# Optimization experiments

Hardware: AMD Instinct MI355X
Metric: run time of the kernel (lower is better)

Reference implementation:

```python
import jax, jax.numpy as jnp
import numpy as np

B, IN, E, H, V, T = 512, 256, 256, 512, 32000, 32


def setup_inputs() -> dict:
    key = jax.random.key(0)
    ks = jax.random.split(key, 8)
    s = 0.05
    return {
        "x": jax.random.normal(ks[0], (B, IN), jnp.float32),
        "agent_w": jax.random.normal(ks[1], (H, IN), jnp.float32) * s,
        "agent_b": jnp.zeros((H,), jnp.float32),
        "sos": jax.random.normal(ks[2], (E,), jnp.float32) * 0.01,
        "emb": jax.random.normal(ks[3], (V, E), jnp.float32) * s,
        "W_ih": jax.random.normal(ks[4], (3 * H, E), jnp.float32) * s,
        "W_hh": jax.random.normal(ks[5], (3 * H, H), jnp.float32) * s,
        "b_ih": jnp.zeros((3 * H,), jnp.float32),
        "b_hh": jnp.zeros((3 * H,), jnp.float32),
        "W_out": jax.random.normal(ks[6], (V, H), jnp.float32) * s,
        "b_out": jnp.zeros((V,), jnp.float32),
        "W_stop": jax.random.normal(ks[7], (1, H), jnp.float32) * s,
        "b_stop": jnp.zeros((1,), jnp.float32),
    }


def _gru_cell(inp, h, W_ih, W_hh, b_ih, b_hh):
    gi = inp @ W_ih.T + b_ih              # [B, 3H]
    gh = h @ W_hh.T + b_hh                # [B, 3H]
    i_r, i_z, i_n = jnp.split(gi, 3, axis=1)
    h_r, h_z, h_n = jnp.split(gh, 3, axis=1)
    r = jax.nn.sigmoid(i_r + h_r)
    z = jax.nn.sigmoid(i_z + h_z)
    n = jnp.tanh(i_n + r * h_n)
    return (1.0 - z) * n + z * h


def reference(x, agent_w, agent_b, sos, emb, W_ih, W_hh, b_ih, b_hh,
              W_out, b_out, W_stop, b_stop):
    h0 = x @ agent_w.T + agent_b                       # agent(x) -> [B, H]
    inp0 = jnp.broadcast_to(sos, (x.shape[0], sos.shape[0]))
    keys = jax.random.split(jax.random.key(42), T)

    def step(carry, k):
        h, inp = carry
        h = _gru_cell(inp, h, W_ih, W_hh, b_ih, b_hh)  # noise_scale=0 -> no noise
        symb_logits = h @ W_out.T + b_out              # [B, V]
        stop_logit = (h @ W_stop.T + b_stop)[:, 0]     # [B]
        logp = jax.nn.log_softmax(symb_logits, axis=1)
        k1, k2 = jax.random.split(k)
        symb = jax.random.categorical(k1, symb_logits, axis=1)          # [B] int
        p_stop = jax.nn.sigmoid(stop_logit)
        stop = jax.random.bernoulli(k2, p_stop).astype(jnp.float32)     # [B]
        symb_lp = jnp.take_along_axis(logp, symb[:, None], axis=1)[:, 0]
        # Bernoulli: log p = s - softplus(s), log(1-p) = -softplus(s)
        sp = jax.nn.softplus(stop_logit)
        stop_lp = stop * stop_logit - sp
        symb_ent = -jnp.sum(jnp.exp(logp) * logp, axis=1)
        stop_ent = sp - stop_logit * p_stop
        inp_next = emb[symb]
        return (h, inp_next), (symb, stop, symb_lp, stop_lp, symb_ent, stop_ent)

    _, ys = jax.lax.scan(step, (h0, inp0), keys)
    symb_seq, stop_seq, symb_lp, stop_lp, symb_ent, stop_ent = ys
    # [T, B] -> [B, T]
    tr = lambda a: a.T
    return (tr(symb_seq), tr(stop_seq).astype(jnp.int32),
            tr(symb_lp), tr(stop_lp), tr(symb_ent), tr(stop_ent))
```

## Files before the change

### kernel.cpp

```cpp
#include <hip/hip_runtime.h>
#include <hip/hip_bf16.h>
#include <stdint.h>

#define JAX_PARTITIONABLE 1

#define Bz 512
#define INz 256
#define Ez 256
#define Hz 512
#define Vz 32000
#define Tz 32
#define BTz (Bz * Tz)
#define TINYF 1.17549435e-38f

typedef float otype;
__device__ __forceinline__ void store_out(otype* out, int idx, float v) {
  out[idx] = v;
}

__device__ __forceinline__ uint32_t rotl32(uint32_t x, int r) {
  return (x << r) | (x >> (32 - r));
}
__device__ __forceinline__ void threefry2x32(uint32_t k0, uint32_t k1,
                                             uint32_t x0, uint32_t x1,
                                             uint32_t& o0, uint32_t& o1) {
  const uint32_t ks2 = k0 ^ k1 ^ 0x1BD11BDAu;
  x0 += k0; x1 += k1;
#define TF_R4(a, b, c, d)                              \
  x0 += x1; x1 = rotl32(x1, a); x1 ^= x0;              \
  x0 += x1; x1 = rotl32(x1, b); x1 ^= x0;              \
  x0 += x1; x1 = rotl32(x1, c); x1 ^= x0;              \
  x0 += x1; x1 = rotl32(x1, d); x1 ^= x0;
  TF_R4(13, 15, 26, 6)  x0 += k1;  x1 += ks2 + 1u;
  TF_R4(17, 29, 16, 24) x0 += ks2; x1 += k0 + 2u;
  TF_R4(13, 15, 26, 6)  x0 += k0;  x1 += k1 + 3u;
  TF_R4(17, 29, 16, 24) x0 += k1;  x1 += ks2 + 4u;
  TF_R4(13, 15, 26, 6)  x0 += ks2; x1 += k0 + 5u;
#undef TF_R4
  o0 = x0; o1 = x1;
}
__device__ __forceinline__ uint32_t rand_bits32(uint32_t ka, uint32_t kb,
                                                uint32_t idx, uint32_t n) {
#if JAX_PARTITIONABLE
  (void)n;
  uint32_t o0, o1;
  threefry2x32(ka, kb, 0u, idx, o0, o1);
  return o0 ^ o1;
#else
  uint32_t half = n >> 1;
  uint32_t o0, o1;
  if (idx < half) { threefry2x32(ka, kb, idx, idx + half, o0, o1); return o0; }
  threefry2x32(ka, kb, idx - half, idx, o0, o1); return o1;
#endif
}
__device__ __forceinline__ float bits_to_f01(uint32_t bits) {
  return __uint_as_float((bits >> 9) | 0x3f800000u) - 1.0f;
}

__global__ void RnnSenderReinforce_36799279792759_kernel(otype* __restrict__ out,
                                                         int n, float v) {
  int i = blockIdx.x * 256 + threadIdx.x;
  if (i < n) out[i] = v;
}

__global__ void keys_kernel(uint32_t* __restrict__ keys) {
  int t = threadIdx.x;
  if (t >= Tz) return;
  uint32_t ka, kb;
#if JAX_PARTITIONABLE
  threefry2x32(0u, 42u, 0u, (uint32_t)t, ka, kb);
#else
  {
    uint32_t j0 = 2u * t, j1 = 2u * t + 1u;
    uint32_t a0, a1, b0, b1;
    if (j0 < Tz) { threefry2x32(0u, 42u, j0, j0 + Tz, a0, a1); ka = a0; }
    else         { threefry2x32(0u, 42u, j0 - Tz, j0, a0, a1); ka = a1; }
    if (j1 < Tz) { threefry2x32(0u, 42u, j1, j1 + Tz, b0, b1); kb = b0; }
    else         { threefry2x32(0u, 42u, j1 - Tz, j1, b0, b1); kb = b1; }
  }
#endif
  uint32_t o0, o1;
#if JAX_PARTITIONABLE
  threefry2x32(ka, kb, 0u, 0u, o0, o1);
  keys[t * 4 + 0] = o0; keys[t * 4 + 1] = o1;
  threefry2x32(ka, kb, 0u, 1u, o0, o1);
  keys[t * 4 + 2] = o0; keys[t * 4 + 3] = o1;
#else
  uint32_t p0, p1, q0, q1;
  threefry2x32(ka, kb, 0u, 2u, p0, p1);
  threefry2x32(ka, kb, 1u, 3u, q0, q1);
  keys[t * 4 + 0] = p0; keys[t * 4 + 1] = q0;
  keys[t * 4 + 2] = p1; keys[t * 4 + 3] = q1;
#endif
}

#define GBM 64
#define GBN 64
#define GBK 32
#define LDSS 68

__device__ __forceinline__ void gemm_bt_body(const float* __restrict__ A,
                                             const float* __restrict__ W,
                                             const float* __restrict__ bias,
                                             float* __restrict__ C,
                                             int M, int N, int K,
                                             int bx, int by,
                                             float* As, float* Bs) {
  const int tid = threadIdx.x;
  const int tx = tid & 15;
  const int ty = tid >> 4;
  const int m0 = by * GBM;
  const int n0 = bx * GBN;
  const int lr = tid >> 3;
  const int lc = (tid & 7) << 2;

  float acc[4][4] = {};
  const float* Ap = A + (size_t)(m0 + lr) * K + lc;
  const float* Wp = W + (size_t)(n0 + lr) * K + lc;
  const size_t rstep = (size_t)32 * K;

  for (int k0 = 0; k0 < K; k0 += GBK) {
    float4 a0 = *(const float4*)(Ap + k0);
    float4 a1 = *(const float4*)(Ap + k0 + rstep);
    float4 b0 = *(const float4*)(Wp + k0);
    float4 b1 = *(const float4*)(Wp + k0 + rstep);
    __syncthreads();
    As[(lc + 0) * LDSS + lr] = a0.x;
    As[(lc + 1) * LDSS + lr] = a0.y;
    As[(lc + 2) * LDSS + lr] = a0.z;
    As[(lc + 3) * LDSS + lr] = a0.w;
    As[(lc + 0) * LDSS + lr + 32] = a1.x;
    As[(lc + 1) * LDSS + lr + 32] = a1.y;
    As[(lc + 2) * LDSS + lr + 32] = a1.z;
    As[(lc + 3) * LDSS + lr + 32] = a1.w;
    Bs[(lc + 0) * LDSS + lr] = b0.x;
    Bs[(lc + 1) * LDSS + lr] = b0.y;
    Bs[(lc + 2) * LDSS + lr] = b0.z;
    Bs[(lc + 3) * LDSS + lr] = b0.w;
    Bs[(lc + 0) * LDSS + lr + 32] = b1.x;
    Bs[(lc + 1) * LDSS + lr + 32] = b1.y;
    Bs[(lc + 2) * LDSS + lr + 32] = b1.z;
    Bs[(lc + 3) * LDSS + lr + 32] = b1.w;
    __syncthreads();
#pragma unroll
    for (int kk = 0; kk < GBK; kk++) {
      float4 af = *(const float4*)&As[kk * LDSS + (ty << 2)];
      float4 bf = *(const float4*)&Bs[kk * LDSS + (tx << 2)];
      float ar[4] = {af.x, af.y, af.z, af.w};
      float br[4] = {bf.x, bf.y, bf.z, bf.w};
#pragma unroll
      for (int i = 0; i < 4; i++)
#pragma unroll
        for (int j = 0; j < 4; j++)
          acc[i][j] = fmaf(ar[i], br[j], acc[i][j]);
    }
  }

  const int nc = n0 + (tx << 2);
  float4 bv;
  bv.x = bias[nc + 0]; bv.y = bias[nc + 1]; bv.z = bias[nc + 2]; bv.w = bias[nc + 3];
#pragma unroll
  for (int i = 0; i < 4; i++) {
    int m = m0 + (ty << 2) + i;
    float4 o;
    o.x = acc[i][0] + bv.x;
    o.y = acc[i][1] + bv.y;
    o.z = acc[i][2] + bv.z;
    o.w = acc[i][3] + bv.w;
    *(float4*)(C + (size_t)m * N + nc) = o;
  }
}

__global__ __launch_bounds__(256) void gemm_bt(const float* __restrict__ A,
                                               const float* __restrict__ W,
                                               const float* __restrict__ bias,
                                               float* __restrict__ C,
                                               int M, int N, int K) {
  __shared__ __align__(16) float As[GBK * LDSS];
  __shared__ __align__(16) float Bs[GBK * LDSS];
  gemm_bt_body(A, W, bias, C, M, N, K, blockIdx.x, blockIdx.y, As, Bs);
}

__global__ __launch_bounds__(256) void gru2_kernel(const float* __restrict__ inp,
                                                   const float* __restrict__ Wih,
                                                   const float* __restrict__ bih,
                                                   float* __restrict__ gi,
                                                   const float* __restrict__ h,
                                                   const float* __restrict__ Whh,
                                                   const float* __restrict__ bhh,
                                                   float* __restrict__ gh) {
  __shared__ __align__(16) float As[GBK * LDSS];
  __shared__ __align__(16) float Bs[GBK * LDSS];
  if (blockIdx.z == 0)
    gemm_bt_body(inp, Wih, bih, gi, Bz, 3 * Hz, Ez, blockIdx.x, blockIdx.y, As, Bs);
  else
    gemm_bt_body(h, Whh, bhh, gh, Bz, 3 * Hz, Hz, blockIdx.x, blockIdx.y, As, Bs);
}

#define QBM 256
#define QBN 128
#define QBK 32
#define QLDA 260
#define QLDB 132

__global__ __launch_bounds__(256, 2) void gemm256_bt(const float* __restrict__ A,
                                                     const float* __restrict__ W,
                                                     const float* __restrict__ bias,
                                                     float* __restrict__ C,
                                                     int M, int N, int K) {
  __shared__ __align__(16) float As[QBK * QLDA];
  __shared__ __align__(16) float Bs[QBK * QLDB];
  const int tid = threadIdx.x;
  const int tx = tid & 15;
  const int ty = tid >> 4;

  const int nP = N / QBN;
  const int G = nP >> 3;
  const int lim = G << 4;
  int b = blockIdx.x;
  int P, mi;
  if (b < lim) {
    int g = b >> 4, r = b & 15;
    mi = r >> 3;
    P = (g << 3) + (r & 7);
  } else {
    int e = b - lim;
    P = (G << 3) + (e & 1);
    mi = e >> 1;
  }
  const int m0 = mi * QBM;
  const int n0 = P * QBN;

  const float* Ap = A + (size_t)(m0 + tid) * K;
  const int brr = tid >> 1;
  const int bk = (tid & 1) << 4;
  const float* Wp = W + (size_t)(n0 + brr) * K + bk;

  float4 a[8], bb[4];
#pragma unroll
  for (int j = 0; j < 8; j++) a[j] = *(const float4*)(Ap + j * 4);
#pragma unroll
  for (int j = 0; j < 4; j++) bb[j] = *(const float4*)(Wp + j * 4);

  float acc[16][8] = {};

  for (int k0 = 0; k0 < K; k0 += QBK) {
    __syncthreads();
#pragma unroll
    for (int j = 0; j < 8; j++) {
      As[(j * 4 + 0) * QLDA + tid] = a[j].x;
      As[(j * 4 + 1) * QLDA + tid] = a[j].y;
      As[(j * 4 + 2) * QLDA + tid] = a[j].z;
      As[(j * 4 + 3) * QLDA + tid] = a[j].w;
    }
#pragma unroll
    for (int j = 0; j < 4; j++) {
      Bs[(bk + j * 4 + 0) * QLDB + brr] = bb[j].x;
      Bs[(bk + j * 4 + 1) * QLDB + brr] = bb[j].y;
      Bs[(bk + j * 4 + 2) * QLDB + brr] = bb[j].z;
      Bs[(bk + j * 4 + 3) * QLDB + brr] = bb[j].w;
    }
    __syncthreads();
    if (k0 + QBK < K) {
#pragma unroll
      for (int j = 0; j < 8; j++)
        a[j] = *(const float4*)(Ap + k0 + QBK + j * 4);
#pragma unroll
      for (int j = 0; j < 4; j++)
        bb[j] = *(const float4*)(Wp + k0 + QBK + j * 4);
    }
#pragma unroll 2
    for (int kk = 0; kk < QBK; kk++) {
      const float* Ar = &As[kk * QLDA + (ty << 2)];
      float4 xa0 = *(const float4*)(Ar);
      float4 xa1 = *(const float4*)(Ar + 64);
      float4 xa2 = *(const float4*)(Ar + 128);
      float4 xa3 = *(const float4*)(Ar + 192);
      float4 xb0 = *(const float4*)&Bs[kk * QLDB + (tx << 2)];
      float4 xb1 = *(const float4*)&Bs[kk * QLDB + 64 + (tx << 2)];
      float am[16] = {xa0.x, xa0.y, xa0.z, xa0.w, xa1.x, xa1.y, xa1.z, xa1.w,
                      xa2.x, xa2.y, xa2.z, xa2.w, xa3.x, xa3.y, xa3.z, xa3.w};
      float bn[8] = {xb0.x, xb0.y, xb0.z, xb0.w, xb1.x, xb1.y, xb1.z, xb1.w};
#pragma unroll
      for (int i = 0; i < 16; i++)
#pragma unroll
        for (int j = 0; j < 8; j++)
          acc[i][j] = fmaf(am[i], bn[j], acc[i][j]);
    }
  }

  const int nc0 = n0 + (tx << 2);
  const float4 bv0 = *(const float4*)(bias + nc0);
  const float4 bv1 = *(const float4*)(bias + nc0 + 64);
#pragma unroll
  for (int q = 0; q < 4; q++) {
#pragma unroll
    for (int i = 0; i < 4; i++) {
      const int m = m0 + q * 64 + (ty << 2) + i;
      float* Cp = C + (size_t)m * N + nc0;
      float4 o;
      o.x = acc[q * 4 + i][0] + bv0.x;
      o.y = acc[q * 4 + i][1] + bv0.y;
      o.z = acc[q * 4 + i][2] + bv0.z;
      o.w = acc[q * 4 + i][3] + bv0.w;
      *(float4*)Cp = o;
      float4 o2;
      o2.x = acc[q * 4 + i][4] + bv1.x;
      o2.y = acc[q * 4 + i][5] + bv1.y;
      o2.z = acc[q * 4 + i][6] + bv1.z;
      o2.w = acc[q * 4 + i][7] + bv1.w;
      *(float4*)(Cp + 64) = o2;
    }
  }
}

__global__ __launch_bounds__(512) void gates_stop_kernel(
    const float* __restrict__ gi, const float* __restrict__ gh,
    float* __restrict__ h, const float* __restrict__ W_stop,
    const float* __restrict__ b_stop, const uint32_t* __restrict__ keys,
    int t, otype* __restrict__ out) {
  __shared__ float hrow[Hz];
  const int b = blockIdx.x;
  const int j = threadIdx.x;
  const float* gib = gi + (size_t)b * (3 * Hz);
  const float* ghb = gh + (size_t)b * (3 * Hz);
  float ir = gib[j], iz = gib[j + Hz], in_ = gib[j + 2 * Hz];
  float hr = ghb[j], hz = ghb[j + Hz], hn = ghb[j + 2 * Hz];
  float r = 1.0f / (1.0f + expf(-(ir + hr)));
  float z = 1.0f / (1.0f + expf(-(iz + hz)));
  float n = tanhf(in_ + r * hn);
  float hv = h[(size_t)b * Hz + j];
  float hnew = (1.0f - z) * n + z * hv;
  h[(size_t)b * Hz + j] = hnew;
  hrow[j] = hnew;
  __syncthreads();
  if (j < 64) {
    const int lane = j;
    float s = 0.0f;
    for (int k = lane; k < Hz; k += 64) s = fmaf(hrow[k], W_stop[k], s);
#pragma unroll
    for (int off = 32; off; off >>= 1) s += __shfl_down(s, off, 64);
    if (lane == 0) {
      s += b_stop[0];
      uint32_t bits = rand_bits32(keys[t * 4 + 2], keys[t * 4 + 3], (uint32_t)b, Bz);
      float u = bits_to_f01(bits);
      float p = 1.0f / (1.0f + expf(-s));
      float stop = (u < p) ? 1.0f : 0.0f;
      float sp = fmaxf(s, 0.0f) + log1pf(expf(-fabsf(s)));
      store_out(out, 1 * BTz + b * Tz + t, stop);
      store_out(out, 3 * BTz + b * Tz + t, stop * s - sp);
      store_out(out, 5 * BTz + b * Tz + t, sp - s * p);
    }
  }
}

__global__ __launch_bounds__(256) void sample_kernel(const float* __restrict__ logits,
                                                     const uint32_t* __restrict__ keys,
                                                     int t, otype* __restrict__ out,
                                                     const float* __restrict__ emb,
                                                     float* __restrict__ inp) {
  __shared__ float sm[256], sg[256], sgl[256], sz[256], ss[256];
  __shared__ int sgi[256];
  __shared__ int ssymb;
  const int tid = threadIdx.x;
  const int b = blockIdx.x;
  const float* lb = logits + (size_t)b * Vz;
  const uint32_t k1a = keys[t * 4 + 0], k1b = keys[t * 4 + 1];
  const uint32_t base = (uint32_t)b * (uint32_t)Vz;

  float m = -INFINITY, gbest = -INFINITY, glogit = 0.0f;
  int gidx = 0x7FFFFFFF;
  for (int v = tid; v < Vz; v += 256) {
    float l = lb[v];
    m = fmaxf(m, l);
    uint32_t bits = rand_bits32(k1a, k1b, base + (uint32_t)v, (uint32_t)Bz * Vz);
    float f = bits_to_f01(bits);
    float u = fmaxf(TINYF, f + TINYF);
    float g = -logf(-logf(u));
    float val = l + g;
    if (val > gbest) { gbest = val; gidx = v; glogit = l; }
  }
  sm[tid] = m; sg[tid] = gbest; sgi[tid] = gidx; sgl[tid] = glogit;
  __syncthreads();
  for (int s2 = 128; s2; s2 >>= 1) {
    if (tid < s2) {
      sm[tid] = fmaxf(sm[tid], sm[tid + s2]);
      float go = sg[tid + s2]; int io = sgi[tid + s2];
      if (go > sg[tid] || (go == sg[tid] && io < sgi[tid])) {
        sg[tid] = go; sgi[tid] = io; sgl[tid] = sgl[tid + s2];
      }
    }
    __syncthreads();
  }
  const float M = sm[0];

  float Z = 0.0f, S1 = 0.0f;
  for (int v = tid; v < Vz; v += 256) {
    float sft = lb[v] - M;
    float e = expf(sft);
    Z += e;
    S1 = fmaf(e, sft, S1);
  }
  sz[tid] = Z; ss[tid] = S1;
  __syncthreads();
  for (int s2 = 128; s2; s2 >>= 1) {
    if (tid < s2) { sz[tid] += sz[tid + s2]; ss[tid] += ss[tid + s2]; }
    __syncthreads();
  }
  if (tid == 0) {
    float Zt = sz[0], S1t = ss[0];
    float lse = logf(Zt);
    int symb = sgi[0];
    store_out(out, 0 * BTz + b * Tz + t, (float)symb);
    store_out(out, 2 * BTz + b * Tz + t, (sgl[0] - M) - lse);
    store_out(out, 4 * BTz + b * Tz + t, lse - S1t / Zt);
    ssymb = symb;
  }
  __syncthreads();
  int s = ssymb;
  s = (s < 0) ? 0 : ((s >= Vz) ? (Vz - 1) : s);
  inp[(size_t)b * Ez + tid] = emb[(size_t)s * Ez + tid];
}

__global__ void init_inp_kernel(float* __restrict__ inp, const float* __restrict__ sos) {
  inp[blockIdx.x * Ez + threadIdx.x] = sos[threadIdx.x];
}

extern "C" __attribute__((visibility("default")))
void kernel_launch(void* const* d_in, const int* in_sizes, int n_in,
                   void* d_out, int out_size, void* d_ws, size_t ws_size,
                   hipStream_t stream) {
  const float* x       = (const float*)d_in[0];
  const float* agent_w = (const float*)d_in[1];
  const float* agent_b = (const float*)d_in[2];
  const float* sos     = (const float*)d_in[3];
  const float* emb     = (const float*)d_in[4];
  const float* W_ih    = (const float*)d_in[5];
  const float* W_hh    = (const float*)d_in[6];
  const float* b_ih    = (const float*)d_in[7];
  const float* b_hh    = (const float*)d_in[8];
  const float* W_out   = (const float*)d_in[9];
  const float* b_out   = (const float*)d_in[10];
  const float* W_stop  = (const float*)d_in[11];
  const float* b_stop  = (const float*)d_in[12];
  otype* out = (otype*)d_out;

  float* ws = (float*)d_ws;
  float* h      = ws;
  float* inp    = h + (size_t)Bz * Hz;
  float* gi     = inp + (size_t)Bz * Ez;
  float* gh     = gi + (size_t)Bz * 3 * Hz;
  float* logits = gh + (size_t)Bz * 3 * Hz;
  uint32_t* keys = (uint32_t*)(logits + (size_t)Bz * Vz);

  keys_kernel<<<1, 64, 0, stream>>>(keys);
  init_inp_kernel<<<Bz, Ez, 0, stream>>>(inp, sos);
  gemm_bt<<<dim3(Hz / GBN, Bz / GBM), 256, 0, stream>>>(x, agent_w, agent_b, h,
                                                        Bz, Hz, INz);
  for (int t = 0; t < Tz; t++) {
    gru2_kernel<<<dim3(3 * Hz / GBN, Bz / GBM, 2), 256, 0, stream>>>(
        inp, W_ih, b_ih, gi, h, W_hh, b_hh, gh);
    gates_stop_kernel<<<Bz, 512, 0, stream>>>(gi, gh, h, W_stop, b_stop, keys,
                                              t, out);
    gemm256_bt<<<(Vz / QBN) * (Bz / QBM), 256, 0, stream>>>(h, W_out, b_out,
                                                            logits, Bz, Vz, Hz);
    sample_kernel<<<Bz, 256, 0, stream>>>(logits, keys, t, out, emb, inp);
  }
}
```

Before: 11.12 ms.

## Replace output-projection GEMM with 128x128 double-buffered LDS tile kernel

The vocabulary-projection GEMM moves from 256x128 tiles with 256 threads and 128 accumulators per thread to 128x128 tiles with 512 threads, 32 accumulators per thread, and double-buffered shared memory. The aim is higher occupancy and overlap of global loads and LDS staging with FMA work, using one barrier per K-step. In exchange each block reuses less data from its tile, so more global and LDS traffic flows per FLOP. The block-to-tile swizzle is hardcoded for these problem dimensions.

```diff
diff --git a/kernel.cpp b/kernel.cpp
--- a/kernel.cpp
+++ b/kernel.cpp
@@ -197,120 +197,119 @@
     gemm_bt_body(h, Whh, bhh, gh, Bz, 3 * Hz, Hz, blockIdx.x, blockIdx.y, As, Bs);
 }
 
-#define QBM 256
-#define QBN 128
-#define QBK 32
-#define QLDA 260
-#define QLDB 132
-
-__global__ __launch_bounds__(256, 2) void gemm256_bt(const float* __restrict__ A,
+#define DBM 128
+#define DBN 128
+#define DBK 32
+#define DLD 132
+
+__global__ __launch_bounds__(512, 4) void gemm128_db(const float* __restrict__ A,
                                                      const float* __restrict__ W,
                                                      const float* __restrict__ bias,
                                                      float* __restrict__ C,
                                                      int M, int N, int K) {
-  __shared__ __align__(16) float As[QBK * QLDA];
-  __shared__ __align__(16) float Bs[QBK * QLDB];
+  __shared__ __align__(16) float As[2][DBK * DLD];
+  __shared__ __align__(16) float Bs[2][DBK * DLD];
   const int tid = threadIdx.x;
   const int tx = tid & 15;
   const int ty = tid >> 4;
 
-  const int nP = N / QBN;
-  const int G = nP >> 3;
-  const int lim = G << 4;
   int b = blockIdx.x;
   int P, mi;
-  if (b < lim) {
-    int g = b >> 4, r = b & 15;
+  if (b < 992) {
+    int g = b >> 5, r = b & 31;
     mi = r >> 3;
-    P = (g << 3) + (r & 7);
+    P = g * 8 + (r & 7);
   } else {
-    int e = b - lim;
-    P = (G << 3) + (e & 1);
+    int e = b - 992;
+    P = 248 + (e & 1);
     mi = e >> 1;
   }
-  const int m0 = mi * QBM;
-  const int n0 = P * QBN;
-
-  const float* Ap = A + (size_t)(m0 + tid) * K;
-  const int brr = tid >> 1;
-  const int bk = (tid & 1) << 4;
-  const float* Wp = W + (size_t)(n0 + brr) * K + bk;
-
-  float4 a[8], bb[4];
-#pragma unroll
-  for (int j = 0; j < 8; j++) a[j] = *(const float4*)(Ap + j * 4);
-#pragma unroll
-  for (int j = 0; j < 4; j++) bb[j] = *(const float4*)(Wp + j * 4);
-
-  float acc[16][8] = {};
-
-  for (int k0 = 0; k0 < K; k0 += QBK) {
-    __syncthreads();
-#pragma unroll
-    for (int j = 0; j < 8; j++) {
-      As[(j * 4 + 0) * QLDA + tid] = a[j].x;
-      As[(j * 4 + 1) * QLDA + tid] = a[j].y;
-      As[(j * 4 + 2) * QLDA + tid] = a[j].z;
-      As[(j * 4 + 3) * QLDA + tid] = a[j].w;
+  const int m0 = mi * DBM;
+  const int n0 = P * DBN;
+
+  const int sr = tid >> 2;
+  const int sc = (tid & 3) << 2;
+
+  const float* Ap = A + (size_t)(m0 + sr) * K + sc;
+  const float* Wp = W + (size_t)(n0 + sr) * K + sc;
+
+  float4 a0 = *(const float4*)(Ap);
+  float4 a1 = *(const float4*)(Ap + 16);
+  float4 b0 = *(const float4*)(Wp);
+  float4 b1 = *(const float4*)(Wp + 16);
+
+  float acc[4][8] = {};
+
+#define STAGE_WRITE(buf)                                     \
+  {                                                          \
+    float av0[4] = {a0.x, a0.y, a0.z, a0.w};                 \
+    float av1[4] = {a1.x, a1.y, a1.z, a1.w};                 \
+    float bv0[4] = {b0.x, b0.y, b0.z, b0.w};                 \
+    float bv1[4] = {b1.x, b1.y, b1.z, b1.w};                 \
+    _Pragma("unroll")                                        \
+    for (int j = 0; j < 4; j++) {                            \
+      As[buf][(sc + j) * DLD + sr] = av0[j];                 \
+      Bs[buf][(sc + j) * DLD + sr] = bv0[j];                 \
+      As[buf][(16 + sc + j) * DLD + sr] = av1[j];            \
+      Bs[buf][(16 + sc + j) * DLD + sr] = bv1[j];            \
+    }                                                        \
+  }
+
+  STAGE_WRITE(0);
+  a0 = *(const float4*)(Ap + DBK);
+  a1 = *(const float4*)(Ap + DBK + 16);
+  b0 = *(const float4*)(Wp + DBK);
+  b1 = *(const float4*)(Wp + DBK + 16);
+  __syncthreads();
+
+  for (int k0 = 0; k0 < K; k0 += DBK) {
+    const int cur = (k0 >> 5) & 1;
+    const int nxt = cur ^ 1;
+    if (k0 + DBK < K) {
+      STAGE_WRITE(nxt);
+      if (k0 + 2 * DBK < K) {
+        a0 = *(const float4*)(Ap + k0 + 2 * DBK);
+        a1 = *(const float4*)(Ap + k0 + 2 * DBK + 16);
+        b0 = *(const float4*)(Wp + k0 + 2 * DBK);
+        b1 = *(const float4*)(Wp + k0 + 2 * DBK + 16);
+      }
     }
-#pragma unroll
-    for (int j = 0; j < 4; j++) {
-      Bs[(bk + j * 4 + 0) * QLDB + brr] = bb[j].x;
-      Bs[(bk + j * 4 + 1) * QLDB + brr] = bb[j].y;
-      Bs[(bk + j * 4 + 2) * QLDB + brr] = bb[j].z;
-      Bs[(bk + j * 4 + 3) * QLDB + brr] = bb[j].w;
+#pragma unroll 8
+    for (int kk = 0; kk < DBK; kk++) {
+      float4 af  = *(const float4*)&As[cur][kk * DLD + (ty << 2)];
+      float4 bf0 = *(const float4*)&Bs[cur][kk * DLD + (tx << 2)];
+      float4 bf1 = *(const float4*)&Bs[cur][kk * DLD + 64 + (tx << 2)];
+      float ar[4] = {af.x, af.y, af.z, af.w};
+      float br[8] = {bf0.x, bf0.y, bf0.z, bf0.w, bf1.x, bf1.y, bf1.z, bf1.w};
+#pragma unroll
+      for (int i = 0; i < 4; i++)
+#pragma unroll
+        for (int j = 0; j < 8; j++)
+          acc[i][j] = fmaf(ar[i], br[j], acc[i][j]);
     }
     __syncthreads();
-    if (k0 + QBK < K) {
-#pragma unroll
-      for (int j = 0; j < 8; j++)
-        a[j] = *(const float4*)(Ap + k0 + QBK + j * 4);
-#pragma unroll
-      for (int j = 0; j < 4; j++)
-        bb[j] = *(const float4*)(Wp + k0 + QBK + j * 4);
-    }
-#pragma unroll 2
-    for (int kk = 0; kk < QBK; kk++) {
-      const float* Ar = &As[kk * QLDA + (ty << 2)];
-      float4 xa0 = *(const float4*)(Ar);
-      float4 xa1 = *(const float4*)(Ar + 64);
-      float4 xa2 = *(const float4*)(Ar + 128);
-      float4 xa3 = *(const float4*)(Ar + 192);
-      float4 xb0 = *(const float4*)&Bs[kk * QLDB + (tx << 2)];
-      float4 xb1 = *(const float4*)&Bs[kk * QLDB + 64 + (tx << 2)];
-      float am[16] = {xa0.x, xa0.y, xa0.z, xa0.w, xa1.x, xa1.y, xa1.z, xa1.w,
-                      xa2.x, xa2.y, xa2.z, xa2.w, xa3.x, xa3.y, xa3.z, xa3.w};
-      float bn[8] = {xb0.x, xb0.y, xb0.z, xb0.w, xb1.x, xb1.y, xb1.z, xb1.w};
-#pragma unroll
-      for (int i = 0; i < 16; i++)
-#pragma unroll
-        for (int j = 0; j < 8; j++)
-          acc[i][j] = fmaf(am[i], bn[j], acc[i][j]);
-    }
-  }
+  }
+#undef STAGE_WRITE
 
   const int nc0 = n0 + (tx << 2);
   const float4 bv0 = *(const float4*)(bias + nc0);
   const float4 bv1 = *(const float4*)(bias + nc0 + 64);
 #pragma unroll
-  for (int q = 0; q < 4; q++) {
-#pragma unroll
-    for (int i = 0; i < 4; i++) {
-      const int m = m0 + q * 64 + (ty << 2) + i;
-      float* Cp = C + (size_t)m * N + nc0;
-      float4 o;
-      o.x = acc[q * 4 + i][0] + bv0.x;
-      o.y = acc[q * 4 + i][1] + bv0.y;
-      o.z = acc[q * 4 + i][2] + bv0.z;
-      o.w = acc[q * 4 + i][3] + bv0.w;
-      *(float4*)Cp = o;
-      float4 o2;
-      o2.x = acc[q * 4 + i][4] + bv1.x;
-      o2.y = acc[q * 4 + i][5] + bv1.y;
-      o2.z = acc[q * 4 + i][6] + bv1.z;
-      o2.w = acc[q * 4 + i][7] + bv1.w;
-      *(float4*)(Cp + 64) = o2;
-    }
+  for (int i = 0; i < 4; i++) {
+    const int m = m0 + (ty << 2) + i;
+    float* Cp = C + (size_t)m * N + nc0;
+    float4 o;
+    o.x = acc[i][0] + bv0.x;
+    o.y = acc[i][1] + bv0.y;
+    o.z = acc[i][2] + bv0.z;
+    o.w = acc[i][3] + bv0.w;
+    *(float4*)Cp = o;
+    float4 o2;
+    o2.x = acc[i][4] + bv1.x;
+    o2.y = acc[i][5] + bv1.y;
+    o2.z = acc[i][6] + bv1.z;
+    o2.w = acc[i][7] + bv1.w;
+    *(float4*)(Cp + 64) = o2;
   }
 }
 
@@ -462,7 +461,7 @@
         inp, W_ih, b_ih, gi, h, W_hh, b_hh, gh);
     gates_stop_kernel<<<Bz, 512, 0, stream>>>(gi, gh, h, W_stop, b_stop, keys,
                                               t, out);
-    gemm256_bt<<<(Vz / QBN) * (Bz / QBM), 256, 0, stream>>>(h, W_out, b_out,
+    gemm128_db<<<(Vz / DBN) * (Bz / DBM), 512, 0, stream>>>(h, W_out, b_out,
                                                             logits, Bz, Vz, Hz);
     sample_kernel<<<Bz, 256, 0, stream>>>(logits, keys, t, out, emb, inp);
   }
```

Result: no change. 11.00 ms (-1.0%).
